# Performance work log

Hardware: AMD Instinct MI355X
Metric: run time of the kernel (lower is better)

## Reference

```python
import jax, jax.numpy as jnp
import numpy as np

B, T, I, H, O = 64, 512, 512, 1024, 512
K, N, M = 8, 128, 64  # mem_banks, memory_dims


def setup_inputs() -> dict:
    key = jax.random.key(0)
    ks = jax.random.split(key, 12)
    s = 0.05
    return {
        "x": jax.random.normal(ks[0], (B, T, 1, I), jnp.float32),
        "mem": jax.random.normal(ks[1], (K, N, M), jnp.float32) * s,
        "Wk": jax.random.normal(ks[2], (M, H), jnp.float32) * s,
        "bk": jnp.zeros((M,), jnp.float32),
        "Wri": jax.random.normal(ks[3], (I, M), jnp.float32) * s,  # read_to_in: M*num_reads -> I
        "bri": jnp.zeros((I,), jnp.float32),
        "Wih": jax.random.normal(ks[4], (3 * H, I), jnp.float32) * s,
        "Whh": jax.random.normal(ks[5], (3 * H, H), jnp.float32) * s,
        "bih": jnp.zeros((3 * H,), jnp.float32),
        "bhh": jnp.zeros((3 * H,), jnp.float32),
        "Wout": jax.random.normal(ks[6], (O, H), jnp.float32) * s,
        "bout": jnp.zeros((O,), jnp.float32),
    }


def reference(x, mem, Wk, bk, Wri, bri, Wih, Whh, bih, bhh, Wout, bout):
    b = x.shape[0]
    xt = x.reshape(b, x.shape[1], -1).transpose(1, 0, 2)  # (T, B, I)
    h0 = jnp.zeros((b, Whh.shape[1]), x.dtype)
    mem_flat = mem.reshape(-1, mem.shape[-1])  # (K*N, M)

    def step(h, x_t):
        # EMM content-based read over memory banks
        kq = h @ Wk.T + bk                                  # (B, M)
        scores = jnp.einsum('bm,pm->bp', kq, mem_flat)      # (B, K*N)
        w = jax.nn.softmax(scores, axis=-1)
        read = jnp.einsum('bp,pm->bm', w, mem_flat)         # (B, M)
        # controller: relu(read_to_in(read)) added to input, then GRUCell
        r = jax.nn.relu(read @ Wri.T + bri)                 # (B, I)
        xin = x_t + r
        gi = xin @ Wih.T + bih
        gh = h @ Whh.T + bhh
        i_r, i_z, i_n = jnp.split(gi, 3, axis=-1)
        h_r, h_z, h_n = jnp.split(gh, 3, axis=-1)
        rg = jax.nn.sigmoid(i_r + h_r)
        zg = jax.nn.sigmoid(i_z + h_z)
        ng = jnp.tanh(i_n + rg * h_n)
        h_new = (1.0 - zg) * ng + zg * h
        out = jax.nn.sigmoid(h_new @ Wout.T + bout)         # (B, O)
        return h_new, out

    _, outs = jax.lax.scan(step, h0, xt)                    # (T, B, O)
    return outs.transpose(1, 0, 2)                          # (B, T, O)
```

## Files before the change

### kernel.cpp

```cpp
#include <hip/hip_runtime.h>
#include <hip/hip_bf16.h>
#include <hip/hip_fp16.h>


typedef _Float16 half_t;
typedef _Float16 half8 __attribute__((ext_vector_type(8)));
typedef float f32x4 __attribute__((ext_vector_type(4)));

#define NB 64
#define NT 512
#define NI 512
#define NH 1024
#define G3 3072
#define NP 1024
#define NM 64
#define HB (NB * NH)
#define MTP 1032

#define NGH 96
#define NGI 32
#define NEMM 64
#define GRID (NGH + NGI + NEMM)

__device__ __forceinline__ float sigm(float v) { return 1.f / (1.f + __expf(-v)); }

union SM {
    half_t ghw[32 * 1024];
    half_t giw[96 * 512];
    struct {
        half_t memT[NM * MTP];
        half_t w16[NP];
        float  kqs[NM];
        float  rd[NM];
        float  red[512];
        float  mred[8], sred[8];
    } e;
};

__device__ __forceinline__ void gbar(unsigned* bar, unsigned bidx) {
    __syncthreads();
    if (threadIdx.x == 0) {
        unsigned* cnt = bar;
        unsigned* gen = bar + 32;
        unsigned a = __hip_atomic_fetch_add(cnt, 1u, __ATOMIC_RELAXED, __HIP_MEMORY_SCOPE_AGENT);
        if (a == bidx * GRID - 1u) {
            __hip_atomic_store(gen, bidx, __ATOMIC_RELAXED, __HIP_MEMORY_SCOPE_AGENT);
        } else {
            while (__hip_atomic_load(gen, __ATOMIC_RELAXED, __HIP_MEMORY_SCOPE_AGENT) < bidx) {
                __builtin_amdgcn_s_sleep(4);
            }
        }
    }
    __syncthreads();
}

__global__ __launch_bounds__(256) void prep_kernel(
    const float* __restrict__ Whh, const float* __restrict__ Wih,
    const float* __restrict__ Wout, const float* __restrict__ mem,
    const float* __restrict__ Wk, const float* __restrict__ Wri,
    half_t* __restrict__ Whh_fm, half_t* __restrict__ Wih_fm,
    half_t* __restrict__ Wout16, half_t* __restrict__ memT16p,
    half_t* __restrict__ Wk16, half_t* __restrict__ Wri16,
    half_t* __restrict__ hist0, float* __restrict__ h32,
    unsigned* __restrict__ bar)
{
    size_t stride = (size_t)gridDim.x * blockDim.x;
    size_t t0 = (size_t)blockIdx.x * blockDim.x + threadIdx.x;
    for (size_t i = t0; i < (size_t)3145728; i += stride) {
        unsigned w = (unsigned)i & 32767u;
        int g = (int)(i >> 15);
        int ct = w >> 14, r = w & 16383;
        int kk = r >> 9, u = r & 511;
        int e = u & 7, rr = (u >> 3) & 15, kg = u >> 7;
        int srow = g * 32 + ct * 16 + rr, scol = kk * 32 + kg * 8 + e;
        Whh_fm[i] = (half_t)Whh[(size_t)srow * NH + scol];
    }
    for (size_t i = t0; i < (size_t)1572864; i += stride) {
        int gb = (int)(i / 49152);
        int w = (int)(i % 49152);
        int gt = w / 16384, r = w & 16383;
        int ct = r >> 13, r2 = r & 8191;
        int kk = r2 >> 9, u = r2 & 511;
        int e = u & 7, rr = (u >> 3) & 15, kg = u >> 7;
        int srow = gt * NH + gb * 32 + ct * 16 + rr, scol = kk * 32 + kg * 8 + e;
        Wih_fm[i] = (half_t)Wih[(size_t)srow * NI + scol];
    }
    for (size_t i = t0; i < (size_t)NI * NH; i += stride) Wout16[i] = (half_t)Wout[i];
    for (size_t i = t0; i < (size_t)NP * NM; i += stride) {
        int p = (int)(i >> 6), m = (int)(i & 63);
        memT16p[(size_t)m * MTP + p] = (half_t)mem[i];
    }
    for (size_t i = t0; i < (size_t)NM * NH; i += stride) Wk16[i] = (half_t)Wk[i];
    for (size_t i = t0; i < (size_t)NI * NM; i += stride) Wri16[i] = (half_t)Wri[i];
    for (size_t i = t0; i < (size_t)HB; i += stride) hist0[i] = (half_t)0.f;
    for (size_t i = t0; i < (size_t)2 * HB; i += stride) h32[i] = 0.f;
    if (t0 < 64) bar[t0] = 0u;
}

__global__ __launch_bounds__(512) void ntm_persist(
    half_t* __restrict__ hist, float* __restrict__ h32,
    const half_t* __restrict__ Whh_fm, const float* __restrict__ bhh,
    float* __restrict__ gh32,
    const half_t* __restrict__ Wih_fm, const float* __restrict__ bih,
    const float* __restrict__ x,
    const half_t* __restrict__ memT16p,
    const half_t* __restrict__ Wk16, const float* __restrict__ bk,
    const half_t* __restrict__ Wri16, const float* __restrict__ bri,
    half_t* __restrict__ xinR,
    unsigned* __restrict__ bar)
{
    __shared__ SM sm;
    const int bid = blockIdx.x, tid = threadIdx.x;

    if (bid < NGH) {
        const uint4* s = (const uint4*)(Whh_fm + (size_t)bid * 32768);
        uint4* d = (uint4*)sm.ghw;
        for (int i = tid; i < 4096; i += 512) d[i] = s[i];
    } else if (bid < NGH + NGI) {
        const uint4* s = (const uint4*)(Wih_fm + (size_t)(bid - NGH) * 49152);
        uint4* d = (uint4*)sm.giw;
        for (int i = tid; i < 6144; i += 512) d[i] = s[i];
    } else {
        const uint4* s = (const uint4*)memT16p;
        uint4* d = (uint4*)sm.e.memT;
        for (int i = tid; i < 8256; i += 512) d[i] = s[i];
    }
    __syncthreads();

    const int wv = tid >> 6, lane = tid & 63;
    const int mt = wv & 3, ct = wv >> 2;
    const int row = lane & 15, kg = lane >> 4;
    unsigned bidx = 0;

    for (int t = 0; t < NT; ++t) {
        float* hprev = h32 + (size_t)(t & 1) * HB;
        float* hnext = h32 + (size_t)((t + 1) & 1) * HB;
        half_t* xin = xinR + (size_t)t * (NB * NI);

        if (bid < NGH) {
            const half_t* ap = hist + (size_t)t * HB + (size_t)(mt * 16 + row) * NH + kg * 8;
            const half_t* bl = sm.ghw + ct * 16384 + (kg * 16 + row) * 8;
            f32x4 acc = {0.f, 0.f, 0.f, 0.f};
#pragma unroll
            for (int kk = 0; kk < 32; ++kk)
                acc = __builtin_amdgcn_mfma_f32_16x16x32_f16(
                    *(const half8*)(ap + kk * 32), *(const half8*)(bl + kk * 512), acc, 0, 0, 0);
            int n = bid * 32 + ct * 16 + row;
            float bb = bhh[n];
#pragma unroll
            for (int r = 0; r < 4; ++r)
                __hip_atomic_store(&gh32[(size_t)(mt * 16 + kg * 4 + r) * G3 + n],
                                   acc[r] + bb, __ATOMIC_RELAXED, __HIP_MEMORY_SCOPE_AGENT);
        } else if (bid >= NGH + NGI) {
            const int b = bid - (NGH + NGI);
            float xv = x[((size_t)b * NT + t) * NI + tid];
            const int m = tid & 63, q = tid >> 6;
            {
                const half_t* hp = hist + (size_t)t * HB + (size_t)b * NH + q * 128;
                const half_t* wk = Wk16 + (size_t)m * NH + q * 128;
                float s = 0.f;
#pragma unroll
                for (int j = 0; j < 128; j += 8) {
                    half8 hv = *(const half8*)(hp + j);
                    half8 wvv = *(const half8*)(wk + j);
#pragma unroll
                    for (int e2 = 0; e2 < 8; ++e2) s += (float)hv[e2] * (float)wvv[e2];
                }
                sm.e.red[tid] = s;
            }
            __syncthreads();
            if (tid < 64) {
                float s = bk[tid];
#pragma unroll
                for (int q2 = 0; q2 < 8; ++q2) s += sm.e.red[q2 * 64 + tid];
                sm.e.kqs[tid] = s;
            }
            __syncthreads();
            float s0 = 0.f, s1 = 0.f;
            {
                const half_t* mp0 = sm.e.memT + tid * 2;
#pragma unroll 8
                for (int m2 = 0; m2 < 64; ++m2) {
                    float km = sm.e.kqs[m2];
                    const half_t* mp = mp0 + m2 * MTP;
                    s0 += km * (float)mp[0];
                    s1 += km * (float)mp[1];
                }
            }
            float lmax = fmaxf(s0, s1);
            for (int o = 32; o; o >>= 1) lmax = fmaxf(lmax, __shfl_xor(lmax, o));
            if ((tid & 63) == 0) sm.e.mred[tid >> 6] = lmax;
            __syncthreads();
            float gmax = sm.e.mred[0];
#pragma unroll
            for (int q2 = 1; q2 < 8; ++q2) gmax = fmaxf(gmax, sm.e.mred[q2]);
            float e0 = __expf(s0 - gmax), e1 = __expf(s1 - gmax);
            float ls = e0 + e1;
            for (int o = 32; o; o >>= 1) ls += __shfl_xor(ls, o);
            if ((tid & 63) == 0) sm.e.sred[tid >> 6] = ls;
            sm.e.w16[tid * 2] = (half_t)e0;
            sm.e.w16[tid * 2 + 1] = (half_t)e1;
            __syncthreads();
            float wsum = 0.f;
#pragma unroll
            for (int q2 = 0; q2 < 8; ++q2) wsum += sm.e.sred[q2];
            float winv = 1.f / wsum;
            {
                const half_t* mp = sm.e.memT + m * MTP + q * 128;
                const half_t* wp = sm.e.w16 + q * 128;
                float s = 0.f;
#pragma unroll
                for (int p0 = 0; p0 < 128; p0 += 8) {
                    half8 mv = *(const half8*)(mp + p0);
                    half8 wv2 = *(const half8*)(wp + p0);
#pragma unroll
                    for (int e2 = 0; e2 < 8; ++e2) s += (float)mv[e2] * (float)wv2[e2];
                }
                sm.e.red[tid] = s;
            }
            __syncthreads();
            if (tid < 64) {
                float s = 0.f;
#pragma unroll
                for (int q2 = 0; q2 < 8; ++q2) s += sm.e.red[q2 * 64 + tid];
                sm.e.rd[tid] = s * winv;
            }
            __syncthreads();
            {
                const half_t* wr = Wri16 + (size_t)tid * NM;
                float s = bri[tid];
#pragma unroll
                for (int m2 = 0; m2 < 64; m2 += 8) {
                    half8 wv2 = *(const half8*)(wr + m2);
#pragma unroll
                    for (int e2 = 0; e2 < 8; ++e2) s += sm.e.rd[m2 + e2] * (float)wv2[e2];
                }
                s = fmaxf(s, 0.f) + xv;
                unsigned short u = __builtin_bit_cast(unsigned short, (half_t)s);
                unsigned short un = (unsigned short)__shfl_xor((int)u, 1);
                if ((tid & 1) == 0) {
                    unsigned pack = (unsigned)u | ((unsigned)un << 16);
                    __hip_atomic_store((unsigned*)&xin[(size_t)b * NI + tid], pack,
                                       __ATOMIC_RELAXED, __HIP_MEMORY_SCOPE_AGENT);
                }
            }
        }
        gbar(bar, ++bidx);

        if (bid >= NGH && bid < NGH + NGI) {
            const int gb = bid - NGH;
            const half_t* ap = xin + (size_t)(mt * 16 + row) * NI + kg * 8;
            const half_t* bR = sm.giw + ct * 8192 + (kg * 16 + row) * 8;
            const half_t* bZ = bR + 16384;
            const half_t* bN = bR + 32768;
            f32x4 aR = {0.f,0.f,0.f,0.f}, aZ = {0.f,0.f,0.f,0.f}, aN = {0.f,0.f,0.f,0.f};
#pragma unroll
            for (int kk = 0; kk < 16; ++kk) {
                half8 a = *(const half8*)(ap + kk * 32);
                aR = __builtin_amdgcn_mfma_f32_16x16x32_f16(a, *(const half8*)(bR + kk * 512), aR, 0, 0, 0);
                aZ = __builtin_amdgcn_mfma_f32_16x16x32_f16(a, *(const half8*)(bZ + kk * 512), aZ, 0, 0, 0);
                aN = __builtin_amdgcn_mfma_f32_16x16x32_f16(a, *(const half8*)(bN + kk * 512), aN, 0, 0, 0);
            }
            int n = gb * 32 + ct * 16 + row;
            float biR = bih[n], biZ = bih[NH + n], biN = bih[2 * NH + n];
#pragma unroll
            for (int r = 0; r < 4; ++r) {
                int b2 = mt * 16 + kg * 4 + r;
                float ghr = __hip_atomic_load(&gh32[(size_t)b2 * G3 + n],
                                              __ATOMIC_RELAXED, __HIP_MEMORY_SCOPE_AGENT);
                float ghz = __hip_atomic_load(&gh32[(size_t)b2 * G3 + NH + n],
                                              __ATOMIC_RELAXED, __HIP_MEMORY_SCOPE_AGENT);
                float ghn = __hip_atomic_load(&gh32[(size_t)b2 * G3 + 2 * NH + n],
                                              __ATOMIC_RELAXED, __HIP_MEMORY_SCOPE_AGENT);
                float rg = sigm(aR[r] + biR + ghr);
                float zg = sigm(aZ[r] + biZ + ghz);
                float ng = tanhf(aN[r] + biN + rg * ghn);
                float hp = hprev[(size_t)b2 * NH + n];
                float hn = (1.f - zg) * ng + zg * hp;
                hnext[(size_t)b2 * NH + n] = hn;
                unsigned short u = __builtin_bit_cast(unsigned short, (half_t)hn);
                unsigned short un = (unsigned short)__shfl_xor((int)u, 1);
                if ((row & 1) == 0) {
                    unsigned pack = (unsigned)u | ((unsigned)un << 16);
                    __hip_atomic_store((unsigned*)&hist[(size_t)(t + 1) * HB + (size_t)b2 * NH + n],
                                       pack, __ATOMIC_RELAXED, __HIP_MEMORY_SCOPE_AGENT);
                }
            }
        }
        gbar(bar, ++bidx);
    }
}

__global__ __launch_bounds__(256) void out_kernel(
    const half_t* __restrict__ hist,
    const half_t* __restrict__ Wout16,
    const float* __restrict__ bout,
    float* __restrict__ out)
{
    int tid = threadIdx.x;
    int widx = tid >> 6, lane = tid & 63;
    int m0 = blockIdx.x * 64 + widx * 16;
    int row = lane & 15, kg = lane >> 4;
    const half_t* ap = hist + HB + (size_t)(m0 + row) * NH + kg * 8;
    for (int ctl = 0; ctl < 32; ++ctl) {
        int n0 = ctl * 16;
        const half_t* bp = Wout16 + (size_t)(n0 + row) * NH + kg * 8;
        f32x4 acc = {0.f, 0.f, 0.f, 0.f};
#pragma unroll
        for (int kk = 0; kk < 32; ++kk) {
            acc = __builtin_amdgcn_mfma_f32_16x16x32_f16(
                *(const half8*)(ap + kk * 32), *(const half8*)(bp + kk * 32), acc, 0, 0, 0);
        }
        int n = n0 + row;
        float bo = bout[n];
#pragma unroll
        for (int r = 0; r < 4; ++r) {
            int m = m0 + kg * 4 + r;
            int b2 = m & 63, tt = m >> 6;
            out[((size_t)b2 * NT + tt) * NI + n] = sigm(acc[r] + bo);
        }
    }
}

extern "C" void kernel_launch(void* const* d_in, const int* in_sizes, int n_in,
                              void* d_out, int out_size, void* d_ws, size_t ws_size,
                              hipStream_t stream) {
    const float* x    = (const float*)d_in[0];
    const float* mem  = (const float*)d_in[1];
    const float* Wk   = (const float*)d_in[2];
    const float* bk   = (const float*)d_in[3];
    const float* Wri  = (const float*)d_in[4];
    const float* bri  = (const float*)d_in[5];
    const float* Wih  = (const float*)d_in[6];
    const float* Whh  = (const float*)d_in[7];
    const float* bih  = (const float*)d_in[8];
    const float* bhh  = (const float*)d_in[9];
    const float* Wout = (const float*)d_in[10];
    const float* bout = (const float*)d_in[11];
    float* out = (float*)d_out;

    size_t off = 0;
    char* wsb = (char*)d_ws;
    auto carve = [&](size_t bytes) -> char* {
        char* p = wsb + off;
        off += (bytes + 255) & ~(size_t)255;
        return p;
    };
    half_t* Whh_fm  = (half_t*)carve((size_t)G3 * NH * 2);
    half_t* Wih_fm  = (half_t*)carve((size_t)G3 * NI * 2);
    half_t* Wout16  = (half_t*)carve((size_t)NI * NH * 2);
    half_t* memT16p = (half_t*)carve((size_t)NM * MTP * 2);
    half_t* Wk16    = (half_t*)carve((size_t)NM * NH * 2);
    half_t* Wri16   = (half_t*)carve((size_t)NI * NM * 2);
    half_t* hist    = (half_t*)carve((size_t)(NT + 1) * HB * 2);
    float*  h32     = (float*)carve((size_t)2 * HB * 4);
    float*  gh32    = (float*)carve((size_t)NB * G3 * 4);
    unsigned* bar   = (unsigned*)carve(256);
    half_t* xinR    = (half_t*)carve((size_t)NT * NB * NI * 2);
    (void)ws_size; (void)in_sizes; (void)n_in; (void)out_size;

    prep_kernel<<<dim3(2048), dim3(256), 0, stream>>>(
        Whh, Wih, Wout, mem, Wk, Wri,
        Whh_fm, Wih_fm, Wout16, memT16p, Wk16, Wri16, hist, h32, bar);

    ntm_persist<<<dim3(GRID), dim3(512), 0, stream>>>(
        hist, h32, Whh_fm, bhh, gh32, Wih_fm, bih, x,
        memT16p, Wk16, bk, Wri16, bri, xinR, bar);

    out_kernel<<<dim3(512), dim3(256), 0, stream>>>(hist, Wout16, bout, out);
}
```

Baseline: 11.03 ms.

## Replace full grid barriers with split producer/consumer hierarchical barriers

Replaces the two all-block grid barriers per timestep with asymmetric arrive/wait barriers. The 160 producer blocks (GH and EMM) arrive on one of 8 group counters, and the last arrival in each group bumps a shared counter, so contention on a single atomic is reduced. Only the 32 GI consumer blocks wait on that counter. The producers then wait only on the GI blocks' completion counter. This removes blocks from waits they do not need and shortens the critical path of each step, at the cost of more intricate ordering that relies on relaxed atomics for visibility.

```diff
diff --git a/kernel.cpp b/kernel.cpp
--- a/kernel.cpp
+++ b/kernel.cpp
@@ -21,6 +21,9 @@
 #define NGI 32
 #define NEMM 64
 #define GRID (NGH + NGI + NEMM)
+
+#define B1_GROUPS 8
+#define B1_PER_GROUP 20
 
 __device__ __forceinline__ float sigm(float v) { return 1.f / (1.f + __expf(-v)); }
 
@@ -37,19 +40,33 @@
     } e;
 };
 
-__device__ __forceinline__ void gbar(unsigned* bar, unsigned bidx) {
+__device__ __forceinline__ void bar1_arrive(unsigned* bar, int arr_idx, unsigned ep) {
     __syncthreads();
     if (threadIdx.x == 0) {
-        unsigned* cnt = bar;
-        unsigned* gen = bar + 32;
-        unsigned a = __hip_atomic_fetch_add(cnt, 1u, __ATOMIC_RELAXED, __HIP_MEMORY_SCOPE_AGENT);
-        if (a == bidx * GRID - 1u) {
-            __hip_atomic_store(gen, bidx, __ATOMIC_RELAXED, __HIP_MEMORY_SCOPE_AGENT);
-        } else {
-            while (__hip_atomic_load(gen, __ATOMIC_RELAXED, __HIP_MEMORY_SCOPE_AGENT) < bidx) {
-                __builtin_amdgcn_s_sleep(4);
-            }
-        }
+        unsigned* grp = bar + 64 + (arr_idx / B1_PER_GROUP) * 32;
+        unsigned a = __hip_atomic_fetch_add(grp, 1u, __ATOMIC_RELAXED, __HIP_MEMORY_SCOPE_AGENT);
+        if (a == ep * B1_PER_GROUP - 1u)
+            __hip_atomic_fetch_add(bar + 32, 1u, __ATOMIC_RELAXED, __HIP_MEMORY_SCOPE_AGENT);
+    }
+}
+__device__ __forceinline__ void bar1_wait(unsigned* bar, unsigned ep) {
+    if (threadIdx.x == 0) {
+        while (__hip_atomic_load(bar + 32, __ATOMIC_RELAXED, __HIP_MEMORY_SCOPE_AGENT)
+               < ep * B1_GROUPS)
+            __builtin_amdgcn_s_sleep(2);
+    }
+    __syncthreads();
+}
+__device__ __forceinline__ void bar2_arrive(unsigned* bar) {
+    __syncthreads();
+    if (threadIdx.x == 0)
+        __hip_atomic_fetch_add(bar, 1u, __ATOMIC_RELAXED, __HIP_MEMORY_SCOPE_AGENT);
+}
+__device__ __forceinline__ void bar2_wait(unsigned* bar, unsigned ep) {
+    if (threadIdx.x == 0) {
+        while (__hip_atomic_load(bar, __ATOMIC_RELAXED, __HIP_MEMORY_SCOPE_AGENT)
+               < ep * NGI)
+            __builtin_amdgcn_s_sleep(2);
     }
     __syncthreads();
 }
@@ -94,7 +111,7 @@
     for (size_t i = t0; i < (size_t)NI * NM; i += stride) Wri16[i] = (half_t)Wri[i];
     for (size_t i = t0; i < (size_t)HB; i += stride) hist0[i] = (half_t)0.f;
     for (size_t i = t0; i < (size_t)2 * HB; i += stride) h32[i] = 0.f;
-    if (t0 < 64) bar[t0] = 0u;
+    if (t0 < 512) bar[t0] = 0u;
 }
 
 __global__ __launch_bounds__(512) void ntm_persist(
@@ -130,9 +147,10 @@
     const int wv = tid >> 6, lane = tid & 63;
     const int mt = wv & 3, ct = wv >> 2;
     const int row = lane & 15, kg = lane >> 4;
-    unsigned bidx = 0;
+    const int arr_idx = (bid < NGH) ? bid : (bid - NGI);
 
     for (int t = 0; t < NT; ++t) {
+        const unsigned ep = (unsigned)(t + 1);
         float* hprev = h32 + (size_t)(t & 1) * HB;
         float* hnext = h32 + (size_t)((t + 1) & 1) * HB;
         half_t* xin = xinR + (size_t)t * (NB * NI);
@@ -151,6 +169,8 @@
             for (int r = 0; r < 4; ++r)
                 __hip_atomic_store(&gh32[(size_t)(mt * 16 + kg * 4 + r) * G3 + n],
                                    acc[r] + bb, __ATOMIC_RELAXED, __HIP_MEMORY_SCOPE_AGENT);
+            bar1_arrive(bar, arr_idx, ep);
+            bar2_wait(bar, ep);
         } else if (bid >= NGH + NGI) {
             const int b = bid - (NGH + NGI);
             float xv = x[((size_t)b * NT + t) * NI + tid];
@@ -244,10 +264,10 @@
                                        __ATOMIC_RELAXED, __HIP_MEMORY_SCOPE_AGENT);
                 }
             }
-        }
-        gbar(bar, ++bidx);
-
-        if (bid >= NGH && bid < NGH + NGI) {
+            bar1_arrive(bar, arr_idx, ep);
+            bar2_wait(bar, ep);
+        } else {
+            bar1_wait(bar, ep);
             const int gb = bid - NGH;
             const half_t* ap = xin + (size_t)(mt * 16 + row) * NI + kg * 8;
             const half_t* bR = sm.giw + ct * 8192 + (kg * 16 + row) * 8;
@@ -286,8 +306,8 @@
                                        pack, __ATOMIC_RELAXED, __HIP_MEMORY_SCOPE_AGENT);
                 }
             }
+            bar2_arrive(bar);
         }
-        gbar(bar, ++bidx);
     }
 }
 
@@ -355,7 +375,7 @@
     half_t* hist    = (half_t*)carve((size_t)(NT + 1) * HB * 2);
     float*  h32     = (float*)carve((size_t)2 * HB * 4);
     float*  gh32    = (float*)carve((size_t)NB * G3 * 4);
-    unsigned* bar   = (unsigned*)carve(256);
+    unsigned* bar   = (unsigned*)carve(2048);
     half_t* xinR    = (half_t*)carve((size_t)NT * NB * NI * 2);
     (void)ws_size; (void)in_sizes; (void)n_in; (void)out_size;
 
```

Result: slower. 11.53 ms (+4.5%).
